# Kernel tuning notes

Hardware: AMD Instinct MI355X
Metric: run time of the kernel (lower is better)

## Reference

```python
import jax, jax.numpy as jnp
import numpy as np

N, D = 1024, 512
BS, N_TEXT, N_VIDEO = 64, 16, 16
BETA = 1.0
N_ITERS = 50


def setup_inputs() -> dict:
    key = jax.random.key(0)
    k1, k2 = jax.random.split(key)
    return {
        "t_prob": jax.random.normal(k1, (N, D), dtype=jnp.float32),
        "v_prob": jax.random.normal(k2, (N, D), dtype=jnp.float32),
        "n": N,
        "bs": BS,
        "n_text": N_TEXT,
        "n_video": N_VIDEO,
    }


def _l2norm(x):
    # matches F.normalize(x, p=2, dim=1) (eps irrelevant for randn inputs)
    return x / jnp.linalg.norm(x, axis=1, keepdims=True)


def reference(t_prob, v_prob, n, bs, n_text, n_video):
    dt = t_prob.dtype
    x = _l2norm(t_prob)
    y = _l2norm(v_prob)
    C = 1.0 - x @ y.T                      # [n, n] cosine distance
    A = jnp.exp(-C / BETA)

    sigma0 = jnp.ones((n, 1), dtype=dt) / n
    T0 = jnp.ones((n, n), dtype=dt)

    def step(carry, _):
        T, sigma = carry
        Q = A * T                          # [n, n]
        delta = 1.0 / (n * (Q @ sigma))    # [n, 1]
        sigma_new = 1.0 / (n * (Q.T @ delta))  # [n, 1]
        # diag(delta) @ Q @ diag(sigma) == row/col rescale
        T_new = delta * Q * sigma_new.T
        return (T_new, sigma_new), None

    (T, _), _ = jax.lax.scan(step, (T0, sigma0), None, length=N_ITERS)

    distance_matrix = C.T @ T              # [n, n]
    distance_matrix = distance_matrix.reshape(bs, n_text, bs, n_video).mean(axis=(1, 3))
    dis_loss = jnp.trace(distance_matrix)
    return distance_matrix, dis_loss
```

## Files before the change

### kernel.cpp

```cpp
#include <hip/hip_runtime.h>
#include <math.h>


#define NWG 32
#define TPB 256
#define NIT 50
#define NREP 4

typedef unsigned long long ull;

constexpr int CL_OFF   = 0;
constexpr int CVEC_OFF = 1024 * 1024;
constexpr int CNT_OFF  = CVEC_OFF + 3 * NREP * 1024;

__global__ __launch_bounds__(256) void k_gemm(const float* __restrict__ X,
                                              const float* __restrict__ Y,
                                              float* __restrict__ ws) {
    __shared__ float As[32][68];
    __shared__ float Bs[32][68];
    __shared__ float nX[64], nY[64];
    float* Cl = ws + CL_OFF;

    int tid = threadIdx.x;
    int tx = tid & 15, ty = tid >> 4;
    int bx = blockIdx.x, by = blockIdx.y;
    int lr0 = tid >> 3;
    int kq  = (tid & 7) * 4;

    float acc[4][4] = {};
    float sx0 = 0.f, sx1 = 0.f, sy0 = 0.f, sy1 = 0.f;
    for (int k0 = 0; k0 < 512; k0 += 32) {
        float4 xa = *(const float4*)(X + (size_t)(by * 64 + lr0) * 512 + k0 + kq);
        float4 xb = *(const float4*)(X + (size_t)(by * 64 + lr0 + 32) * 512 + k0 + kq);
        float4 ya = *(const float4*)(Y + (size_t)(bx * 64 + lr0) * 512 + k0 + kq);
        float4 yb = *(const float4*)(Y + (size_t)(bx * 64 + lr0 + 32) * 512 + k0 + kq);
        sx0 += xa.x * xa.x + xa.y * xa.y + xa.z * xa.z + xa.w * xa.w;
        sx1 += xb.x * xb.x + xb.y * xb.y + xb.z * xb.z + xb.w * xb.w;
        sy0 += ya.x * ya.x + ya.y * ya.y + ya.z * ya.z + ya.w * ya.w;
        sy1 += yb.x * yb.x + yb.y * yb.y + yb.z * yb.z + yb.w * yb.w;
        As[kq + 0][lr0] = xa.x; As[kq + 1][lr0] = xa.y;
        As[kq + 2][lr0] = xa.z; As[kq + 3][lr0] = xa.w;
        As[kq + 0][lr0 + 32] = xb.x; As[kq + 1][lr0 + 32] = xb.y;
        As[kq + 2][lr0 + 32] = xb.z; As[kq + 3][lr0 + 32] = xb.w;
        Bs[kq + 0][lr0] = ya.x; Bs[kq + 1][lr0] = ya.y;
        Bs[kq + 2][lr0] = ya.z; Bs[kq + 3][lr0] = ya.w;
        Bs[kq + 0][lr0 + 32] = yb.x; Bs[kq + 1][lr0 + 32] = yb.y;
        Bs[kq + 2][lr0 + 32] = yb.z; Bs[kq + 3][lr0 + 32] = yb.w;
        __syncthreads();
#pragma unroll
        for (int kk = 0; kk < 32; ++kk) {
            float4 a4 = *(const float4*)&As[kk][4 * ty];
            float4 b4 = *(const float4*)&Bs[kk][4 * tx];
            float av[4] = {a4.x, a4.y, a4.z, a4.w};
            float bv[4] = {b4.x, b4.y, b4.z, b4.w};
#pragma unroll
            for (int r = 0; r < 4; ++r)
#pragma unroll
                for (int q = 0; q < 4; ++q) acc[r][q] += av[r] * bv[q];
        }
        __syncthreads();
    }
#pragma unroll
    for (int m = 1; m < 8; m <<= 1) {
        sx0 += __shfl_xor(sx0, m, 64);
        sx1 += __shfl_xor(sx1, m, 64);
        sy0 += __shfl_xor(sy0, m, 64);
        sy1 += __shfl_xor(sy1, m, 64);
    }
    if ((tid & 7) == 0) {
        nX[lr0] = sx0; nX[lr0 + 32] = sx1;
        nY[lr0] = sy0; nY[lr0 + 32] = sy1;
    }
    __syncthreads();

    int i0 = by * 64 + 4 * ty, j0 = bx * 64 + 4 * tx;
    float vy[4];
#pragma unroll
    for (int q = 0; q < 4; ++q) vy[q] = 1.0f / sqrtf(nY[4 * tx + q]);
#pragma unroll
    for (int r = 0; r < 4; ++r) {
        float vx = 1.0f / sqrtf(nX[4 * ty + r]);
        float4 o;
        o.x = acc[r][0] * vx * vy[0] - 1.0f;
        o.y = acc[r][1] * vx * vy[1] - 1.0f;
        o.z = acc[r][2] * vx * vy[2] - 1.0f;
        o.w = acc[r][3] * vx * vy[3] - 1.0f;
        *(float4*)(Cl + (size_t)(i0 + r) * 1024 + j0) = o;
    }
}

__device__ __forceinline__ float f_lo(ull u) { return __uint_as_float((unsigned)u); }
__device__ __forceinline__ float f_hi(ull u) { return __uint_as_float((unsigned)(u >> 32)); }

__device__ __forceinline__ void wavepoll(const unsigned* cnt, int lane,
                                         unsigned tgt) {
    int done = (lane < 4)
        ? (__hip_atomic_load(&cnt[lane * 32], __ATOMIC_RELAXED,
                             __HIP_MEMORY_SCOPE_AGENT) >= tgt) : 1;
    long gd = 0;
    while (!__all(done)) {
        __builtin_amdgcn_s_sleep(1);
        if (lane < 4)
            done = (__hip_atomic_load(&cnt[lane * 32], __ATOMIC_RELAXED,
                                      __HIP_MEMORY_SCOPE_AGENT) >= tgt);
        if (++gd > 2000000) break;
    }
}

__global__ __launch_bounds__(256, 1) void k_ipot(float* __restrict__ ws,
                                                 float* __restrict__ out) {
    __shared__ float rws[4][32];
    __shared__ float aLs[32];
    __shared__ float PsRs[4096];
    __shared__ float twv[4];

    const int g = blockIdx.x, tid = threadIdx.x;
    const int rs = tid >> 6, lane = tid & 63;
    const int j0 = rs * 256 + lane * 4;
    float* Cl   = ws + CL_OFF;
    float* cvec = ws + CVEC_OFF;
    unsigned* cnt = (unsigned*)(ws + CNT_OFF);

    float E1[32][4], E[32][4], Pp[32];
#pragma unroll
    for (int i = 0; i < 32; ++i) {
        float4 c = *(const float4*)(Cl + (size_t)(g * 32 + i) * 1024 + j0);
        Pp[i] = c.x + c.y + c.z + c.w;
        E1[i][0] = __expf(c.x); E1[i][1] = __expf(c.y);
        E1[i][2] = __expf(c.z); E1[i][3] = __expf(c.w);
        E[i][0] = E1[i][0]; E[i][1] = E1[i][1];
        E[i][2] = E1[i][2]; E[i][3] = E1[i][3];
    }
    float bv[4] = {1.0f, 1.0f, 1.0f, 1.0f};
    float al[32];

    for (int t = 0; t < NIT; ++t) {
        float s0, s1, s2, s3;
        if (t == 0) {
            s0 = s1 = s2 = s3 = 1.0f / 1024.0f;
        } else {
            wavepoll(cnt, lane, (unsigned)t * 8u);
            const ull* rb = (const ull*)(cvec + ((t + 2) % 3) * (NREP * 1024)) + (j0 >> 1);
            ull a0 = __hip_atomic_load(rb + 0,    __ATOMIC_RELAXED, __HIP_MEMORY_SCOPE_AGENT);
            ull a1 = __hip_atomic_load(rb + 1,    __ATOMIC_RELAXED, __HIP_MEMORY_SCOPE_AGENT);
            ull b0 = __hip_atomic_load(rb + 512,  __ATOMIC_RELAXED, __HIP_MEMORY_SCOPE_AGENT);
            ull b1 = __hip_atomic_load(rb + 513,  __ATOMIC_RELAXED, __HIP_MEMORY_SCOPE_AGENT);
            ull c0 = __hip_atomic_load(rb + 1024, __ATOMIC_RELAXED, __HIP_MEMORY_SCOPE_AGENT);
            ull c1 = __hip_atomic_load(rb + 1025, __ATOMIC_RELAXED, __HIP_MEMORY_SCOPE_AGENT);
            ull d0 = __hip_atomic_load(rb + 1536, __ATOMIC_RELAXED, __HIP_MEMORY_SCOPE_AGENT);
            ull d1 = __hip_atomic_load(rb + 1537, __ATOMIC_RELAXED, __HIP_MEMORY_SCOPE_AGENT);
            if (t >= 2 && tid < 64) {
                ull* zb = (ull*)(cvec + ((t + 1) % 3) * (NREP * 1024)) + g * 64 + tid;
                __hip_atomic_store(zb, 0ull, __ATOMIC_RELAXED, __HIP_MEMORY_SCOPE_AGENT);
            }
            float cc0 = f_lo(a0) + f_lo(b0) + f_lo(c0) + f_lo(d0);
            float cc1 = f_hi(a0) + f_hi(b0) + f_hi(c0) + f_hi(d0);
            float cc2 = f_lo(a1) + f_lo(b1) + f_lo(c1) + f_lo(d1);
            float cc3 = f_hi(a1) + f_hi(b1) + f_hi(c1) + f_hi(d1);
            float nb0 = 1.0f / cc0, nb1 = 1.0f / cc1;
            float nb2 = 1.0f / cc2, nb3 = 1.0f / cc3;
            s0 = nb0 * nb0 / bv[0] * (1.0f / 1024.0f); bv[0] = nb0;
            s1 = nb1 * nb1 / bv[1] * (1.0f / 1024.0f); bv[1] = nb1;
            s2 = nb2 * nb2 / bv[2] * (1.0f / 1024.0f); bv[2] = nb2;
            s3 = nb3 * nb3 / bv[3] * (1.0f / 1024.0f); bv[3] = nb3;
        }

        float v[32];
#pragma unroll
        for (int i = 0; i < 32; ++i)
            v[i] = E[i][0] * s0 + E[i][1] * s1 + E[i][2] * s2 + E[i][3] * s3;
#pragma unroll
        for (int st = 0; st < 5; ++st) {
            const int m = 1 << st;
            const bool up = (lane & m) != 0;
#pragma unroll
            for (int i = 0; i < (16 >> st); ++i) {
                float x = v[2 * i], y = v[2 * i + 1];
                float send = up ? x : y;
                float keep = up ? y : x;
                v[i] = keep + __shfl_xor(send, m, 64);
            }
        }
        v[0] += __shfl_xor(v[0], 32, 64);
        if (lane < 32) rws[rs][lane] = v[0];
        __syncthreads();
        if (tid < 32)
            aLs[tid] = 1.0f / (1024.0f * (rws[0][tid] + rws[1][tid] +
                                          rws[2][tid] + rws[3][tid]));
        __syncthreads();
#pragma unroll
        for (int q = 0; q < 8; ++q) {
            float4 a4 = *(const float4*)&aLs[4 * q];
            al[4*q] = a4.x; al[4*q+1] = a4.y; al[4*q+2] = a4.z; al[4*q+3] = a4.w;
        }

        float p0 = 0.f, p1 = 0.f, p2 = 0.f, p3 = 0.f;
#pragma unroll
        for (int i = 0; i < 32; ++i) {
            float ai = al[i];
            p0 += E[i][0] * ai; p1 += E[i][1] * ai;
            p2 += E[i][2] * ai; p3 += E[i][3] * ai;
        }
        float* wb = cvec + (t % 3) * (NREP * 1024) + (g & 3) * 1024 + j0;
        atomicAdd(wb + 0, p0);
        atomicAdd(wb + 1, p1);
        atomicAdd(wb + 2, p2);
        atomicAdd(wb + 3, p3);

        if (t < NIT - 1) {
#pragma unroll
            for (int i = 0; i < 32; ++i) {
                E[i][0] *= E1[i][0]; E[i][1] *= E1[i][1];
                E[i][2] *= E1[i][2]; E[i][3] *= E1[i][3];
            }
        }
        __syncthreads();
        if (tid == 0)
            __hip_atomic_fetch_add(&cnt[(g >> 3) * 32], 1u, __ATOMIC_RELAXED,
                                   __HIP_MEMORY_SCOPE_AGENT);
    }

    wavepoll(cnt, lane, (unsigned)NIT * 8u);
    float bl[4];
    {
        const ull* rb = (const ull*)(cvec + ((NIT - 1) % 3) * (NREP * 1024)) + (j0 >> 1);
        ull a0 = __hip_atomic_load(rb + 0,    __ATOMIC_RELAXED, __HIP_MEMORY_SCOPE_AGENT);
        ull a1 = __hip_atomic_load(rb + 1,    __ATOMIC_RELAXED, __HIP_MEMORY_SCOPE_AGENT);
        ull b0 = __hip_atomic_load(rb + 512,  __ATOMIC_RELAXED, __HIP_MEMORY_SCOPE_AGENT);
        ull b1 = __hip_atomic_load(rb + 513,  __ATOMIC_RELAXED, __HIP_MEMORY_SCOPE_AGENT);
        ull c0 = __hip_atomic_load(rb + 1024, __ATOMIC_RELAXED, __HIP_MEMORY_SCOPE_AGENT);
        ull c1 = __hip_atomic_load(rb + 1025, __ATOMIC_RELAXED, __HIP_MEMORY_SCOPE_AGENT);
        ull d0 = __hip_atomic_load(rb + 1536, __ATOMIC_RELAXED, __HIP_MEMORY_SCOPE_AGENT);
        ull d1 = __hip_atomic_load(rb + 1537, __ATOMIC_RELAXED, __HIP_MEMORY_SCOPE_AGENT);
        bl[0] = 1.0f / (f_lo(a0) + f_lo(b0) + f_lo(c0) + f_lo(d0));
        bl[1] = 1.0f / (f_hi(a0) + f_hi(b0) + f_hi(c0) + f_hi(d0));
        bl[2] = 1.0f / (f_lo(a1) + f_lo(b1) + f_lo(c1) + f_lo(d1));
        bl[3] = 1.0f / (f_hi(a1) + f_hi(b1) + f_hi(c1) + f_hi(d1));
    }

    float* Ps = PsRs;
    float* Rs = PsRs + 2048;
    float Pl[32], Rl[32];
#pragma unroll
    for (int k = 0; k < 32; ++k) {
        Pl[k] = Pp[k];
        Rl[k] = E[k][0] * bl[0] + E[k][1] * bl[1] +
                E[k][2] * bl[2] + E[k][3] * bl[3];
    }
#pragma unroll
    for (int m = 1; m < 4; m <<= 1)
#pragma unroll
        for (int k = 0; k < 32; ++k) {
            Pl[k] += __shfl_xor(Pl[k], m, 64);
            Rl[k] += __shfl_xor(Rl[k], m, 64);
        }
    if ((lane & 3) == 0) {
        int A = rs * 16 + (lane >> 2);
#pragma unroll
        for (int k = 0; k < 32; ++k) {
            Ps[k * 64 + A] = -Pl[k];
            Rs[k * 64 + A] = al[k] * Rl[k];
        }
    }
    __syncthreads();

    float Rk[32];
#pragma unroll
    for (int k = 0; k < 32; ++k) Rk[k] = Rs[k * 64 + lane];
    const float sc = 1.0f / (256.0f * 1024.0f);
    float tsum = 0.0f;
#pragma unroll
    for (int q = 0; q < 16; ++q) {
        int o = tid + 256 * q;
        int A = 4 * q + rs;
        float acc = 0.0f;
#pragma unroll
        for (int k = 0; k < 32; ++k) acc += Ps[k * 64 + A] * Rk[k];
        float val = acc * sc;
        atomicAdd(out + o, val);
        if (A == lane) tsum += val;
    }
#pragma unroll
    for (int m = 1; m < 64; m <<= 1) tsum += __shfl_xor(tsum, m, 64);
    if (lane == 0) twv[rs] = tsum;
    __syncthreads();
    if (tid == 0) atomicAdd(out + 4096, twv[0] + twv[1] + twv[2] + twv[3]);
}

extern "C" void kernel_launch(void* const* d_in, const int* in_sizes, int n_in,
                              void* d_out, int out_size, void* d_ws, size_t ws_size,
                              hipStream_t stream) {
    const float* X = (const float*)d_in[0];
    const float* Y = (const float*)d_in[1];
    float* out = (float*)d_out;
    float* ws  = (float*)d_ws;

    (void)hipMemsetAsync((char*)d_ws + (size_t)CVEC_OFF * 4, 0,
                         (3 * NREP * 1024 + 128) * 4, stream);
    (void)hipMemsetAsync(d_out, 0, (size_t)out_size * 4, stream);

    k_gemm<<<dim3(16, 16), 256, 0, stream>>>(X, Y, ws);
    k_ipot<<<NWG, TPB, 0, stream>>>(ws, out);
}
```

Baseline: 346.8 us.

## Replace global counter barrier with per-element value/count pair polling

```diff
diff --git a/kernel.cpp b/kernel.cpp
--- a/kernel.cpp
+++ b/kernel.cpp
@@ -10,8 +10,8 @@
 typedef unsigned long long ull;
 
 constexpr int CL_OFF   = 0;
-constexpr int CVEC_OFF = 1024 * 1024;
-constexpr int CNT_OFF  = CVEC_OFF + 3 * NREP * 1024;
+constexpr int PAIR_OFF = 1024 * 1024;
+constexpr int PAIR_BUF = NREP * 1024 * 2;
 
 __global__ __launch_bounds__(256) void k_gemm(const float* __restrict__ X,
                                               const float* __restrict__ Y,
@@ -90,20 +90,29 @@
 }
 
 __device__ __forceinline__ float f_lo(ull u) { return __uint_as_float((unsigned)u); }
-__device__ __forceinline__ float f_hi(ull u) { return __uint_as_float((unsigned)(u >> 32)); }
-
-__device__ __forceinline__ void wavepoll(const unsigned* cnt, int lane,
-                                         unsigned tgt) {
-    int done = (lane < 4)
-        ? (__hip_atomic_load(&cnt[lane * 32], __ATOMIC_RELAXED,
-                             __HIP_MEMORY_SCOPE_AGENT) >= tgt) : 1;
+
+__device__ __forceinline__ void pairpoll(const ull* pb, int j0, float* cc) {
     long gd = 0;
-    while (!__all(done)) {
+    for (;;) {
+        float c0 = 0.f, c1 = 0.f, c2 = 0.f, c3 = 0.f;
+        int mine = 1;
+#pragma unroll
+        for (int r = 0; r < 4; ++r) {
+            ull u0 = __hip_atomic_load(pb + r * 1024 + j0 + 0, __ATOMIC_RELAXED, __HIP_MEMORY_SCOPE_AGENT);
+            ull u1 = __hip_atomic_load(pb + r * 1024 + j0 + 1, __ATOMIC_RELAXED, __HIP_MEMORY_SCOPE_AGENT);
+            ull u2 = __hip_atomic_load(pb + r * 1024 + j0 + 2, __ATOMIC_RELAXED, __HIP_MEMORY_SCOPE_AGENT);
+            ull u3 = __hip_atomic_load(pb + r * 1024 + j0 + 3, __ATOMIC_RELAXED, __HIP_MEMORY_SCOPE_AGENT);
+            mine &= ((unsigned)(u0 >> 32) == 0x41000000u);
+            mine &= ((unsigned)(u1 >> 32) == 0x41000000u);
+            mine &= ((unsigned)(u2 >> 32) == 0x41000000u);
+            mine &= ((unsigned)(u3 >> 32) == 0x41000000u);
+            c0 += f_lo(u0); c1 += f_lo(u1); c2 += f_lo(u2); c3 += f_lo(u3);
+        }
+        if (__all(mine) || ++gd > 500000) {
+            cc[0] = c0; cc[1] = c1; cc[2] = c2; cc[3] = c3;
+            return;
+        }
         __builtin_amdgcn_s_sleep(1);
-        if (lane < 4)
-            done = (__hip_atomic_load(&cnt[lane * 32], __ATOMIC_RELAXED,
-                                      __HIP_MEMORY_SCOPE_AGENT) >= tgt);
-        if (++gd > 2000000) break;
     }
 }
 
@@ -117,9 +126,8 @@
     const int g = blockIdx.x, tid = threadIdx.x;
     const int rs = tid >> 6, lane = tid & 63;
     const int j0 = rs * 256 + lane * 4;
-    float* Cl   = ws + CL_OFF;
-    float* cvec = ws + CVEC_OFF;
-    unsigned* cnt = (unsigned*)(ws + CNT_OFF);
+    float* Cl    = ws + CL_OFF;
+    float* pairs = ws + PAIR_OFF;
 
     float E1[32][4], E[32][4], Pp[32];
 #pragma unroll
@@ -139,26 +147,14 @@
         if (t == 0) {
             s0 = s1 = s2 = s3 = 1.0f / 1024.0f;
         } else {
-            wavepoll(cnt, lane, (unsigned)t * 8u);
-            const ull* rb = (const ull*)(cvec + ((t + 2) % 3) * (NREP * 1024)) + (j0 >> 1);
-            ull a0 = __hip_atomic_load(rb + 0,    __ATOMIC_RELAXED, __HIP_MEMORY_SCOPE_AGENT);
-            ull a1 = __hip_atomic_load(rb + 1,    __ATOMIC_RELAXED, __HIP_MEMORY_SCOPE_AGENT);
-            ull b0 = __hip_atomic_load(rb + 512,  __ATOMIC_RELAXED, __HIP_MEMORY_SCOPE_AGENT);
-            ull b1 = __hip_atomic_load(rb + 513,  __ATOMIC_RELAXED, __HIP_MEMORY_SCOPE_AGENT);
-            ull c0 = __hip_atomic_load(rb + 1024, __ATOMIC_RELAXED, __HIP_MEMORY_SCOPE_AGENT);
-            ull c1 = __hip_atomic_load(rb + 1025, __ATOMIC_RELAXED, __HIP_MEMORY_SCOPE_AGENT);
-            ull d0 = __hip_atomic_load(rb + 1536, __ATOMIC_RELAXED, __HIP_MEMORY_SCOPE_AGENT);
-            ull d1 = __hip_atomic_load(rb + 1537, __ATOMIC_RELAXED, __HIP_MEMORY_SCOPE_AGENT);
-            if (t >= 2 && tid < 64) {
-                ull* zb = (ull*)(cvec + ((t + 1) % 3) * (NREP * 1024)) + g * 64 + tid;
+            float cc[4];
+            pairpoll((const ull*)(pairs + ((t + 2) % 3) * PAIR_BUF), j0, cc);
+            if (tid < 128) {
+                ull* zb = (ull*)(pairs + ((t + 1) % 3) * PAIR_BUF) + g * 128 + tid;
                 __hip_atomic_store(zb, 0ull, __ATOMIC_RELAXED, __HIP_MEMORY_SCOPE_AGENT);
             }
-            float cc0 = f_lo(a0) + f_lo(b0) + f_lo(c0) + f_lo(d0);
-            float cc1 = f_hi(a0) + f_hi(b0) + f_hi(c0) + f_hi(d0);
-            float cc2 = f_lo(a1) + f_lo(b1) + f_lo(c1) + f_lo(d1);
-            float cc3 = f_hi(a1) + f_hi(b1) + f_hi(c1) + f_hi(d1);
-            float nb0 = 1.0f / cc0, nb1 = 1.0f / cc1;
-            float nb2 = 1.0f / cc2, nb3 = 1.0f / cc3;
+            float nb0 = 1.0f / cc[0], nb1 = 1.0f / cc[1];
+            float nb2 = 1.0f / cc[2], nb3 = 1.0f / cc[3];
             s0 = nb0 * nb0 / bv[0] * (1.0f / 1024.0f); bv[0] = nb0;
             s1 = nb1 * nb1 / bv[1] * (1.0f / 1024.0f); bv[1] = nb1;
             s2 = nb2 * nb2 / bv[2] * (1.0f / 1024.0f); bv[2] = nb2;
@@ -201,11 +197,11 @@
             p0 += E[i][0] * ai; p1 += E[i][1] * ai;
             p2 += E[i][2] * ai; p3 += E[i][3] * ai;
         }
-        float* wb = cvec + (t % 3) * (NREP * 1024) + (g & 3) * 1024 + j0;
-        atomicAdd(wb + 0, p0);
-        atomicAdd(wb + 1, p1);
-        atomicAdd(wb + 2, p2);
-        atomicAdd(wb + 3, p3);
+        float* vb = pairs + (t % 3) * PAIR_BUF + (g & 3) * 2048 + 2 * j0;
+        atomicAdd(vb + 0, p0);
+        atomicAdd(vb + 2, p1);
+        atomicAdd(vb + 4, p2);
+        atomicAdd(vb + 6, p3);
 
         if (t < NIT - 1) {
 #pragma unroll
@@ -215,27 +211,18 @@
             }
         }
         __syncthreads();
-        if (tid == 0)
-            __hip_atomic_fetch_add(&cnt[(g >> 3) * 32], 1u, __ATOMIC_RELAXED,
-                                   __HIP_MEMORY_SCOPE_AGENT);
-    }
-
-    wavepoll(cnt, lane, (unsigned)NIT * 8u);
+        atomicAdd(vb + 1, 1.0f);
+        atomicAdd(vb + 3, 1.0f);
+        atomicAdd(vb + 5, 1.0f);
+        atomicAdd(vb + 7, 1.0f);
+    }
+
     float bl[4];
     {
-        const ull* rb = (const ull*)(cvec + ((NIT - 1) % 3) * (NREP * 1024)) + (j0 >> 1);
-        ull a0 = __hip_atomic_load(rb + 0,    __ATOMIC_RELAXED, __HIP_MEMORY_SCOPE_AGENT);
-        ull a1 = __hip_atomic_load(rb + 1,    __ATOMIC_RELAXED, __HIP_MEMORY_SCOPE_AGENT);
-        ull b0 = __hip_atomic_load(rb + 512,  __ATOMIC_RELAXED, __HIP_MEMORY_SCOPE_AGENT);
-        ull b1 = __hip_atomic_load(rb + 513,  __ATOMIC_RELAXED, __HIP_MEMORY_SCOPE_AGENT);
-        ull c0 = __hip_atomic_load(rb + 1024, __ATOMIC_RELAXED, __HIP_MEMORY_SCOPE_AGENT);
-        ull c1 = __hip_atomic_load(rb + 1025, __ATOMIC_RELAXED, __HIP_MEMORY_SCOPE_AGENT);
-        ull d0 = __hip_atomic_load(rb + 1536, __ATOMIC_RELAXED, __HIP_MEMORY_SCOPE_AGENT);
-        ull d1 = __hip_atomic_load(rb + 1537, __ATOMIC_RELAXED, __HIP_MEMORY_SCOPE_AGENT);
-        bl[0] = 1.0f / (f_lo(a0) + f_lo(b0) + f_lo(c0) + f_lo(d0));
-        bl[1] = 1.0f / (f_hi(a0) + f_hi(b0) + f_hi(c0) + f_hi(d0));
-        bl[2] = 1.0f / (f_lo(a1) + f_lo(b1) + f_lo(c1) + f_lo(d1));
-        bl[3] = 1.0f / (f_hi(a1) + f_hi(b1) + f_hi(c1) + f_hi(d1));
+        float cc[4];
+        pairpoll((const ull*)(pairs + ((NIT - 1) % 3) * PAIR_BUF), j0, cc);
+        bl[0] = 1.0f / cc[0]; bl[1] = 1.0f / cc[1];
+        bl[2] = 1.0f / cc[2]; bl[3] = 1.0f / cc[3];
     }
 
     float* Ps = PsRs;
@@ -295,8 +282,8 @@
     float* out = (float*)d_out;
     float* ws  = (float*)d_ws;
 
-    (void)hipMemsetAsync((char*)d_ws + (size_t)CVEC_OFF * 4, 0,
-                         (3 * NREP * 1024 + 128) * 4, stream);
+    (void)hipMemsetAsync((char*)d_ws + (size_t)PAIR_OFF * 4, 0,
+                         (size_t)3 * PAIR_BUF * 4, stream);
     (void)hipMemsetAsync(d_out, 0, (size_t)out_size * 4, stream);
 
     k_gemm<<<dim3(16, 16), 256, 0, stream>>>(X, Y, ws);
```

Measured after the change: 384.8 us. 10.9% more time.
